# Performance work log

Measured on AMD Instinct MI355X. Metric: run time of the kernel, lower is better.

Reference implementation:

```python
import jax, jax.numpy as jnp
import numpy as np

B = 16384

def _linear_params(key, out_dim, in_dim):
    k1, k2 = jax.random.split(key)
    s = 1.0 / np.sqrt(in_dim)
    W = jax.random.uniform(k1, (out_dim, in_dim), jnp.float32, -s, s)
    b = jax.random.uniform(k2, (out_dim,), jnp.float32, -s, s)
    return W, b

def setup_inputs() -> dict:
    key = jax.random.key(0)
    ks = jax.random.split(key, 6)
    x = jax.random.normal(ks[0], (B, 784), jnp.float32)
    conv_w = jax.random.normal(ks[1], (3, 3), jnp.float32)
    W1, b1 = _linear_params(ks[2], 1024, 26 * 26)
    W2, b2 = _linear_params(ks[3], 512, 1024)
    W3, b3 = _linear_params(ks[4], 256, 512)
    W4, b4 = _linear_params(ks[5], 10, 256)
    return {"x": x, "conv_w": conv_w, "W1": W1, "b1": b1, "W2": W2, "b2": b2,
            "W3": W3, "b3": b3, "W4": W4, "b4": b4}

def reference(x, conv_w, W1, b1, W2, b2, W3, b3, W4, b4):
    b = x.shape[0]
    img = x.reshape(b, 1, 28, 28)                       # NCHW
    kern = conv_w.reshape(1, 1, 3, 3)                   # OIHW; cross-correlation
    y = jax.lax.conv_general_dilated(img, kern, (1, 1), 'VALID')  # [B,1,26,26]
    h = y.reshape(b, 26 * 26)
    h = jax.nn.relu(h @ W1.T + b1)
    h = jax.nn.relu(h @ W2.T + b2)
    h = jax.nn.relu(h @ W3.T + b3)
    return h @ W4.T + b4                                # [B,10] logits
```

## Files before the change

### kernel.cpp

```cpp
#include <hip/hip_runtime.h>
#include <hip/hip_bf16.h>
#include <stdint.h>

#define BDIM 256

typedef __attribute__((ext_vector_type(8))) short short8;
typedef __attribute__((ext_vector_type(4))) float f32x4;

#define AS1 __attribute__((address_space(1)))
#define AS3 __attribute__((address_space(3)))
#define GLL16(g, s) __builtin_amdgcn_global_load_lds((AS1 const void*)(g), (AS3 void*)(s), 16, 0, 0)

__device__ __forceinline__ unsigned short f2bf(float f) {
  union { float f; unsigned u; } v; v.f = f;
  unsigned r = v.u + 0x7fffu + ((v.u >> 16) & 1u);
  return (unsigned short)(r >> 16);
}
__device__ __forceinline__ float bf2f(unsigned short u) {
  union { unsigned u; float f; } v; v.u = ((unsigned)u) << 16;
  return v.f;
}

__global__ __launch_bounds__(BDIM) void cast_pad_w1(const float* __restrict__ w,
                                                    unsigned short* __restrict__ o) {
  int idx = blockIdx.x * BDIM + threadIdx.x;
  if (idx >= 1024 * 704) return;
  int n = idx / 704, k = idx - n * 704;
  float v = (k < 676) ? w[n * 676 + k] : 0.f;
  o[idx] = f2bf(v);
}

__global__ __launch_bounds__(BDIM) void cast_plain(const float* __restrict__ w,
                                                   unsigned short* __restrict__ o, int count) {
  int idx = blockIdx.x * BDIM + threadIdx.x;
  if (idx < count) o[idx] = f2bf(w[idx]);
}

__global__ __launch_bounds__(BDIM) void conv3x3(const float* __restrict__ x,
                                                const float* __restrict__ cw,
                                                unsigned short* __restrict__ h0) {
  __shared__ float xs[784];
  __shared__ float w[9];
  int m = blockIdx.x;
  const float* xr = x + (size_t)m * 784;
  if (threadIdx.x < 9) w[threadIdx.x] = cw[threadIdx.x];
  for (int i = threadIdx.x; i < 784; i += BDIM) xs[i] = xr[i];
  __syncthreads();
  unsigned short* hr = h0 + (size_t)m * 704;
  for (int p = threadIdx.x; p < 704; p += BDIM) {
    float v = 0.f;
    if (p < 676) {
      int r = p / 26, c = p - r * 26;
      const float* xp = &xs[r * 28 + c];
      v = xp[0]  * w[0] + xp[1]  * w[1] + xp[2]  * w[2]
        + xp[28] * w[3] + xp[29] * w[4] + xp[30] * w[5]
        + xp[56] * w[6] + xp[57] * w[7] + xp[58] * w[8];
    }
    hr[p] = f2bf(v);
  }
}

template <int BM, int BN, int WGM, bool RELU>
__global__ __launch_bounds__(512, 2) void gemm_bt2(const unsigned short* __restrict__ A,
                                                   const unsigned short* __restrict__ Wt,
                                                   const float* __restrict__ bias,
                                                   unsigned short* __restrict__ Cb,
                                                   int M, int N, int K) {
  constexpr int WGN = 8 / WGM;
  constexpr int FM = BM / WGM / 16;
  constexpr int FN = BN / WGN / 16;
  constexpr int RA = BM / 64;
  constexpr int RB = BN / 64;
  __shared__ unsigned short As[2][BM * 64];
  __shared__ unsigned short Bs[2][BN * 64];
  const int tid = threadIdx.x;
  const int lane = tid & 63;
  const int wid = tid >> 6;
  const int nbm = M / BM;
  const int brow = (blockIdx.x % nbm) * BM;
  const int bcol = (blockIdx.x / nbm) * BN;

  const int srow = tid >> 3;
  const int scol = (tid & 7) << 3;
  const unsigned short* gA = A + (size_t)(brow + srow) * K + scol;
  const unsigned short* gB = Wt + (size_t)(bcol + srow) * K + scol;
  const int sdst = tid * 8;

#define STAGE(buf, kt)                                                        \
  do {                                                                        \
    _Pragma("unroll")                                                         \
    for (int r = 0; r < RA; ++r)                                              \
      GLL16(gA + (size_t)r * 64 * K + (kt) * 64, &As[buf][r * 4096 + sdst]);  \
    _Pragma("unroll")                                                         \
    for (int r = 0; r < RB; ++r)                                              \
      GLL16(gB + (size_t)r * 64 * K + (kt) * 64, &Bs[buf][r * 4096 + sdst]);  \
  } while (0)

  f32x4 acc[FM][FN] = {};

  const int fr = lane & 15;
  const int g8 = (lane >> 4) << 3;
  const int abase = (wid / WGN) * (FM * 16);
  const int bbase = (wid % WGN) * (FN * 16);

  const int nk = K >> 6;
  STAGE(0, 0);
  __syncthreads();
  int cur = 0;
  for (int kt = 0; kt < nk; ++kt) {
    if (kt + 1 < nk) STAGE(cur ^ 1, kt + 1);
#pragma unroll
    for (int s = 0; s < 2; ++s) {
      short8 af[FM], bf[FN];
#pragma unroll
      for (int m = 0; m < FM; ++m)
        af[m] = *(const short8*)&As[cur][(abase + m * 16 + fr) * 64 + s * 32 + g8];
#pragma unroll
      for (int n = 0; n < FN; ++n)
        bf[n] = *(const short8*)&Bs[cur][(bbase + n * 16 + fr) * 64 + s * 32 + g8];
#pragma unroll
      for (int m = 0; m < FM; ++m)
#pragma unroll
        for (int n = 0; n < FN; ++n)
          acc[m][n] = __builtin_amdgcn_mfma_f32_16x16x32_bf16(af[m], bf[n], acc[m][n], 0, 0, 0);
    }
    __syncthreads();
    cur ^= 1;
  }
#undef STAGE

  const int crow0 = brow + abase + ((lane >> 4) << 2);
  const int ccol0 = bcol + bbase + fr;
#pragma unroll
  for (int n = 0; n < FN; ++n) {
    const int cc = ccol0 + n * 16;
    const float bv = bias[cc];
#pragma unroll
    for (int m = 0; m < FM; ++m) {
      const int rr = crow0 + m * 16;
#pragma unroll
      for (int j = 0; j < 4; ++j) {
        float v = acc[m][n][j] + bv;
        if (RELU) v = v > 0.f ? v : 0.f;
        Cb[(size_t)(rr + j) * N + cc] = f2bf(v);
      }
    }
  }
}

__global__ __launch_bounds__(BDIM) void fc10(const unsigned short* __restrict__ h3,
                                             const float* __restrict__ W4,
                                             const float* __restrict__ b4,
                                             float* __restrict__ out) {
  int lane = threadIdx.x & 63;
  int wid = threadIdx.x >> 6;
  int m = blockIdx.x * 4 + wid;
  const unsigned short* hr = h3 + (size_t)m * 256 + lane * 4;
  uint64_t hv = *(const uint64_t*)hr;
  float e0 = bf2f((unsigned short)hv), e1 = bf2f((unsigned short)(hv >> 16));
  float e2 = bf2f((unsigned short)(hv >> 32)), e3 = bf2f((unsigned short)(hv >> 48));
#pragma unroll
  for (int n = 0; n < 10; ++n) {
    const float4 wv = *(const float4*)(W4 + n * 256 + lane * 4);
    float s = e0 * wv.x + e1 * wv.y + e2 * wv.z + e3 * wv.w;
#pragma unroll
    for (int off = 32; off > 0; off >>= 1) s += __shfl_xor(s, off);
    if (lane == n) out[(size_t)m * 10 + n] = s + b4[n];
  }
}

extern "C" void kernel_launch(void* const* d_in, const int* in_sizes, int n_in,
                              void* d_out, int out_size, void* d_ws, size_t ws_size,
                              hipStream_t stream) {
  const float* x  = (const float*)d_in[0];
  const float* cw = (const float*)d_in[1];
  const float* W1 = (const float*)d_in[2];
  const float* b1 = (const float*)d_in[3];
  const float* W2 = (const float*)d_in[4];
  const float* b2 = (const float*)d_in[5];
  const float* W3 = (const float*)d_in[6];
  const float* b3 = (const float*)d_in[7];
  const float* W4 = (const float*)d_in[8];
  const float* b4 = (const float*)d_in[9];
  float* out = (float*)d_out;

  char* ws = (char*)d_ws;
  unsigned short* h0  = (unsigned short*)(ws);
  unsigned short* h1  = (unsigned short*)(ws + 23068672);
  unsigned short* W1b = (unsigned short*)(ws + 23068672 + 33554432);
  unsigned short* W2b = W1b + 1024 * 704;
  unsigned short* W3b = W2b + 512 * 1024;
  unsigned short* h2  = h0;
  unsigned short* h3  = h1;

  cast_pad_w1<<<2816, BDIM, 0, stream>>>(W1, W1b);
  cast_plain<<<2048, BDIM, 0, stream>>>(W2, W2b, 512 * 1024);
  cast_plain<<<512, BDIM, 0, stream>>>(W3, W3b, 256 * 512);
  conv3x3<<<16384, BDIM, 0, stream>>>(x, cw, h0);

  gemm_bt2<256, 256, 2, true><<<(16384 / 256) * (1024 / 256), 512, 0, stream>>>(
      h0, W1b, b1, h1, 16384, 1024, 704);
  gemm_bt2<256, 128, 4, true><<<(16384 / 256) * (512 / 128), 512, 0, stream>>>(
      h1, W2b, b2, h2, 16384, 512, 1024);
  gemm_bt2<128, 128, 4, true><<<(16384 / 128) * (256 / 128), 512, 0, stream>>>(
      h2, W3b, b3, h3, 16384, 256, 512);
  fc10<<<16384 / 4, BDIM, 0, stream>>>(h3, W4, b4, out);
}
```

Measured before the change: 135.3 us.

## Swizzle LDS tiles and stage GEMM epilogue through LDS for coalesced stores

Applies an XOR swizzle to the LDS placement of A/B tiles during global-to-LDS loads and the matching fragment reads, to reduce LDS bank conflicts. The epilogue now writes bias+ReLU results into the reused LDS buffer with a swizzle, then writes rows out as 16-byte vectors instead of scattered 2-byte stores. This adds a barrier and an extra LDS round trip in the epilogue.

Measured after the change: 110.1 us. 18.6% less time.

```diff
diff --git a/kernel.cpp b/kernel.cpp
--- a/kernel.cpp
+++ b/kernel.cpp
@@ -71,8 +71,10 @@
   constexpr int FN = BN / WGN / 16;
   constexpr int RA = BM / 64;
   constexpr int RB = BN / 64;
-  __shared__ unsigned short As[2][BM * 64];
-  __shared__ unsigned short Bs[2][BN * 64];
+  __shared__ unsigned short lds[(size_t)(BM + BN) * 128];
+  unsigned short* const Asb = lds;
+  unsigned short* const Bsb = lds + 2 * BM * 64;
+
   const int tid = threadIdx.x;
   const int lane = tid & 63;
   const int wid = tid >> 6;
@@ -81,25 +83,28 @@
   const int bcol = (blockIdx.x / nbm) * BN;
 
   const int srow = tid >> 3;
-  const int scol = (tid & 7) << 3;
-  const unsigned short* gA = A + (size_t)(brow + srow) * K + scol;
-  const unsigned short* gB = Wt + (size_t)(bcol + srow) * K + scol;
+  const int sslot = (tid & 7) ^ (srow & 7);
+  const unsigned short* gA = A + (size_t)(brow + srow) * K + sslot * 8;
+  const unsigned short* gB = Wt + (size_t)(bcol + srow) * K + sslot * 8;
   const int sdst = tid * 8;
 
-#define STAGE(buf, kt)                                                        \
-  do {                                                                        \
-    _Pragma("unroll")                                                         \
-    for (int r = 0; r < RA; ++r)                                              \
-      GLL16(gA + (size_t)r * 64 * K + (kt) * 64, &As[buf][r * 4096 + sdst]);  \
-    _Pragma("unroll")                                                         \
-    for (int r = 0; r < RB; ++r)                                              \
-      GLL16(gB + (size_t)r * 64 * K + (kt) * 64, &Bs[buf][r * 4096 + sdst]);  \
+#define STAGE(buf, kt)                                                            \
+  do {                                                                            \
+    _Pragma("unroll")                                                             \
+    for (int r = 0; r < RA; ++r)                                                  \
+      GLL16(gA + (size_t)r * 64 * K + (size_t)(kt) * 64,                          \
+            Asb + (buf) * BM * 64 + r * 4096 + sdst);                             \
+    _Pragma("unroll")                                                             \
+    for (int r = 0; r < RB; ++r)                                                  \
+      GLL16(gB + (size_t)r * 64 * K + (size_t)(kt) * 64,                          \
+            Bsb + (buf) * BN * 64 + r * 4096 + sdst);                             \
   } while (0)
 
   f32x4 acc[FM][FN] = {};
 
   const int fr = lane & 15;
-  const int g8 = (lane >> 4) << 3;
+  const int h = lane >> 4;
+  const int fx = fr & 7;
   const int abase = (wid / WGN) * (FM * 16);
   const int bbase = (wid % WGN) * (FN * 16);
 
@@ -111,13 +116,14 @@
     if (kt + 1 < nk) STAGE(cur ^ 1, kt + 1);
 #pragma unroll
     for (int s = 0; s < 2; ++s) {
+      const int slot = (((s << 2) + h) ^ fx) << 3;
       short8 af[FM], bf[FN];
 #pragma unroll
       for (int m = 0; m < FM; ++m)
-        af[m] = *(const short8*)&As[cur][(abase + m * 16 + fr) * 64 + s * 32 + g8];
+        af[m] = *(const short8*)&Asb[cur * BM * 64 + (abase + m * 16 + fr) * 64 + slot];
 #pragma unroll
       for (int n = 0; n < FN; ++n)
-        bf[n] = *(const short8*)&Bs[cur][(bbase + n * 16 + fr) * 64 + s * 32 + g8];
+        bf[n] = *(const short8*)&Bsb[cur * BN * 64 + (bbase + n * 16 + fr) * 64 + slot];
 #pragma unroll
       for (int m = 0; m < FM; ++m)
 #pragma unroll
@@ -129,22 +135,33 @@
   }
 #undef STAGE
 
-  const int crow0 = brow + abase + ((lane >> 4) << 2);
-  const int ccol0 = bcol + bbase + fr;
+  unsigned short* const scr = lds;
+  const int lrow0 = abase + (h << 2);
+  const int lcol0 = bbase + fr;
 #pragma unroll
   for (int n = 0; n < FN; ++n) {
-    const int cc = ccol0 + n * 16;
-    const float bv = bias[cc];
+    const int col = lcol0 + n * 16;
+    const float bv = bias[bcol + col];
 #pragma unroll
     for (int m = 0; m < FM; ++m) {
-      const int rr = crow0 + m * 16;
 #pragma unroll
       for (int j = 0; j < 4; ++j) {
+        const int row = lrow0 + m * 16 + j;
         float v = acc[m][n][j] + bv;
         if (RELU) v = v > 0.f ? v : 0.f;
-        Cb[(size_t)(rr + j) * N + cc] = f2bf(v);
+        scr[(row * BN + col) ^ ((row & 12) << 2)] = f2bf(v);
       }
     }
+  }
+  __syncthreads();
+  constexpr int CPR = BN / 8;
+  constexpr int TOT = BM * CPR;
+#pragma unroll 2
+  for (int i = tid; i < TOT; i += 512) {
+    const int row = i / CPR, c = i % CPR;
+    const int cs = c ^ ((row & 12) >> 1);
+    short8 vv = *(const short8*)&scr[row * BN + cs * 8];
+    *(short8*)(Cb + (size_t)(brow + row) * N + bcol + c * 8) = vv;
   }
 }
 
```
